# Performance work log

Hardware: AMD Instinct MI355X
Metric: run time of the kernel (lower is better)

The kernel has to match this reference:

```python
import jax, jax.numpy as jnp
import numpy as np

N = 16000
E = 128000
IN_DIM = 512
H1 = 4096
H2 = 1024
OUT_DIM = 64


def setup_inputs() -> dict:
    key = jax.random.key(0)
    ks = jax.random.split(key, 8)
    x = jax.random.normal(ks[0], (N, IN_DIM), dtype=jnp.float32)
    edge_index = jax.random.randint(ks[1], (2, E), 0, N, dtype=jnp.int64)

    def glorot(k, fan_in, fan_out):
        lim = float(np.sqrt(6.0 / (fan_in + fan_out)))
        return jax.random.uniform(k, (fan_in, fan_out), jnp.float32, -lim, lim)

    # PyG SAGEConv: out = lin_l(mean_j x_j) + lin_r(x); lin_l has bias, lin_r does not.
    params = {
        'W1l': glorot(ks[2], IN_DIM, H1), 'b1': jnp.zeros((H1,), jnp.float32),
        'W1r': glorot(ks[3], IN_DIM, H1),
        'W2l': glorot(ks[4], H1, H2), 'b2': jnp.zeros((H2,), jnp.float32),
        'W2r': glorot(ks[5], H1, H2),
        'W3l': glorot(ks[6], H2, OUT_DIM), 'b3': jnp.zeros((OUT_DIM,), jnp.float32),
        'W3r': glorot(ks[7], H2, OUT_DIM),
    }
    return {'x': x, 'edge_index': edge_index, **params}


def _sage_conv(x, src, dst, Wl, b, Wr):
    # mean-aggregate neighbor features at dst, then linear; plus root transform
    agg = jax.ops.segment_sum(x[src], dst, num_segments=N)          # [N, F_in]
    cnt = jax.ops.segment_sum(jnp.ones((src.shape[0],), x.dtype), dst, num_segments=N)
    mean = agg / jnp.maximum(cnt, 1.0)[:, None]
    return mean @ Wl + b + x @ Wr


def reference(x, edge_index, W1l, b1, W1r, W2l, b2, W2r, W3l, b3, W3r):
    src, dst = edge_index[0], edge_index[1]
    h = jax.nn.relu(_sage_conv(x, src, dst, W1l, b1, W1r))   # dropout is identity in eval
    h = jax.nn.relu(_sage_conv(h, src, dst, W2l, b2, W2r))
    h = _sage_conv(h, src, dst, W3l, b3, W3r)
    return jax.nn.log_softmax(h, axis=1)
```

## Files before the change

### kernel.cpp

```cpp
#include <hip/hip_runtime.h>
#include <stdint.h>

typedef __bf16 bf16x8 __attribute__((ext_vector_type(8)));
typedef float  f32x4  __attribute__((ext_vector_type(4)));
typedef const void __attribute__((address_space(1))) gv_t;
typedef void __attribute__((address_space(3))) sv_t;

static __device__ __forceinline__ unsigned short f2bf(float f) {
  unsigned u = __float_as_uint(f);
  u += 0x7fffu + ((u >> 16) & 1u);
  return (unsigned short)(u >> 16);
}
static __device__ __forceinline__ float bf2f(unsigned short h) {
  return __uint_as_float(((unsigned)h) << 16);
}
static __device__ __forceinline__ void gload16(const void* g, void* l) {
  __builtin_amdgcn_global_load_lds((gv_t*)g, (sv_t*)l, 16, 0, 0);
}

__global__ void k_sentinel(float* out, int n, float val) {
  int t = blockIdx.x * 256 + threadIdx.x;
  if (t < n) out[t] = val;
}
__global__ void k_zero(int* p, int n) {
  int t = blockIdx.x * 256 + threadIdx.x;
  if (t < n) p[t] = 0;
}

__global__ void k_detect(const int* ei, int* flag) {
  if (blockIdx.x == 0 && threadIdx.x == 0) {
    int nz = 0;
    for (int t = 0; t < 256; ++t) nz += (ei[2 * t + 1] != 0);
    *flag = (nz == 0) ? 1 : 0;
  }
}

__global__ void k_degree(const int* ei, int E, const int* flag, int* deg) {
  int t = blockIdx.x * 256 + threadIdx.x;
  if (t < E) {
    int d = (*flag) ? ei[2 * (E + t)] : ei[E + t];
    atomicAdd(&deg[d], 1);
  }
}
__global__ void k_scan(const int* deg, int* rp, int* cur, int n) {
  __shared__ int ssum[256];
  int t = threadIdx.x;
  int chunk = (n + 255) >> 8;
  int lo = t * chunk, hi = min(lo + chunk, n);
  int s = 0;
  for (int i = lo; i < hi; ++i) s += deg[i];
  ssum[t] = s;
  __syncthreads();
  if (t == 0) {
    int run = 0;
    for (int i = 0; i < 256; ++i) { int v = ssum[i]; ssum[i] = run; run += v; }
  }
  __syncthreads();
  int run = ssum[t];
  for (int i = lo; i < hi; ++i) { rp[i] = run; cur[i] = run; run += deg[i]; }
  if (t == 255) rp[n] = run;
}
__global__ void k_fill(const int* ei, int E, const int* flag, int* cur, int* col) {
  int t = blockIdx.x * 256 + threadIdx.x;
  if (t < E) {
    int f = *flag;
    int s = f ? ei[2 * t] : ei[t];
    int d = f ? ei[2 * (E + t)] : ei[E + t];
    int p = atomicAdd(&cur[d], 1);
    col[p] = s;
  }
}

__global__ void k_cvtx(const float4* __restrict__ in, ushort4* __restrict__ xm, int total4) {
  int t = blockIdx.x * 256 + threadIdx.x;
  if (t < total4) {
    int row = t >> 7, c = t & 127;
    float4 v = in[t];
    xm[(size_t)row * 256 + c] = make_ushort4(f2bf(v.x), f2bf(v.y), f2bf(v.z), f2bf(v.w));
  }
}

__global__ void k_transW(const float* W, unsigned short* Wt, int K, int N, int ld, int kofs) {
  __shared__ float tile[32][33];
  int tx = threadIdx.x & 31, ty = threadIdx.x >> 5;
  int n0 = blockIdx.x << 5, k0 = blockIdx.y << 5;
#pragma unroll
  for (int r = 0; r < 4; ++r)
    tile[ty + r * 8][tx] = W[(size_t)(k0 + ty + r * 8) * N + n0 + tx];
  __syncthreads();
#pragma unroll
  for (int r = 0; r < 4; ++r)
    Wt[(size_t)(n0 + ty + r * 8) * ld + kofs + k0 + tx] = f2bf(tile[tx][ty + r * 8]);
}

__global__ void k_agg(ushort4* __restrict__ xm, const int* __restrict__ rp,
                      const int* __restrict__ col) {
  int i = blockIdx.x;
  int s = rp[i], e = rp[i + 1];
  float inv = 1.0f / (float)max(e - s, 1);
  int f = threadIdx.x;
  float4 a = make_float4(0.f, 0.f, 0.f, 0.f);
  for (int n = s; n < e; ++n) {
    ushort4 v = xm[(size_t)col[n] * 256 + f];
    a.x += bf2f(v.x); a.y += bf2f(v.y); a.z += bf2f(v.z); a.w += bf2f(v.w);
  }
  xm[(size_t)i * 256 + 128 + f] =
      make_ushort4(f2bf(a.x * inv), f2bf(a.y * inv), f2bf(a.z * inv), f2bf(a.w * inv));
}

template <bool RELU, bool BIAS>
__global__ __launch_bounds__(512, 1) void k_gemm256(
    const unsigned short* __restrict__ A, const unsigned short* __restrict__ B,
    const float* __restrict__ bias, unsigned short* __restrict__ outp,
    int Mreal, int N, int K, int bnShift) {
  __shared__ __align__(16) unsigned short lds[2][2][256 * 64];

  const int tid = threadIdx.x;
  const int lane = tid & 63;
  const int wq = tid >> 6;
  const int wr = wq >> 2;
  const int wc = wq & 3;

  const int nwg = gridDim.x;
  const int q8 = nwg >> 3, r8 = nwg & 7;
  const int xcd = blockIdx.x & 7, idx = blockIdx.x >> 3;
  const int wg = (xcd < r8 ? xcd * (q8 + 1) : r8 * (q8 + 1) + (xcd - r8) * q8) + idx;
  const int bn = wg & ((1 << bnShift) - 1);
  const int bm = wg >> bnShift;

  const unsigned short* Ap = A + (size_t)bm * 256 * K;
  const unsigned short* Bp = B + (size_t)bn * 256 * K;
  const int sl8 = ((lane & 7) ^ (lane >> 3)) * 8;
  const int rsub = wq * 8 + (lane >> 3);

#define STAGE_A(BUF, I, K0)                                            \
  gload16(Ap + (size_t)((I) * 64 + rsub) * K + (K0) + sl8,             \
          (char*)&lds[BUF][0][0] + ((I) * 64 + wq * 8) * 128)
#define STAGE_B(BUF, I, K0)                                            \
  gload16(Bp + (size_t)((I) * 64 + rsub) * K + (K0) + sl8,             \
          (char*)&lds[BUF][1][0] + ((I) * 64 + wq * 8) * 128)
#define VMCNT(NUM) asm volatile("s_waitcnt vmcnt(" #NUM ")" ::: "memory")

  f32x4 acc[8][4];
#pragma unroll
  for (int m = 0; m < 8; ++m)
#pragma unroll
    for (int n = 0; n < 4; ++n) acc[m][n] = (f32x4){0.f, 0.f, 0.f, 0.f};

#define LOAD_AFR(DST, CUR, QA)                                                          \
  do {                                                                                  \
    const char* baseA = (const char*)&lds[CUR][0][0];                                   \
    _Pragma("unroll") for (int mm = 0; mm < 4; ++mm) {                                  \
      const int rr = ((QA) * 4 + mm) * 32 + wr * 16 + (lane & 15);                      \
      _Pragma("unroll") for (int kk = 0; kk < 2; ++kk)                                  \
          DST[mm][kk] = *(const bf16x8*)(baseA + rr * 128 +                             \
                                         (((kk * 4 + (lane >> 4)) ^ (lane & 7)) << 4)); \
    }                                                                                   \
  } while (0)
#define LOAD_BFR(DST, CUR, QB)                                                          \
  do {                                                                                  \
    const char* baseB = (const char*)&lds[CUR][1][0];                                   \
    _Pragma("unroll") for (int nn = 0; nn < 2; ++nn) {                                  \
      const int cc = ((QB) * 2 + nn) * 64 + wc * 16 + (lane & 15);                      \
      _Pragma("unroll") for (int kk = 0; kk < 2; ++kk)                                  \
          DST[nn][kk] = *(const bf16x8*)(baseB + cc * 128 +                             \
                                         (((kk * 4 + (lane >> 4)) ^ (lane & 7)) << 4)); \
    }                                                                                   \
  } while (0)
#define MFMA_Q(QA, QB, AFR, BFR)                                                        \
  do {                                                                                  \
    _Pragma("unroll") for (int mm = 0; mm < 4; ++mm)                                    \
        _Pragma("unroll") for (int nn = 0; nn < 2; ++nn)                                \
            _Pragma("unroll") for (int kk = 0; kk < 2; ++kk)                            \
                acc[(QA) * 4 + mm][(QB) * 2 + nn] =                                     \
                    __builtin_amdgcn_mfma_f32_16x16x32_bf16(                            \
                        AFR[mm][kk], BFR[nn][kk], acc[(QA) * 4 + mm][(QB) * 2 + nn],    \
                        0, 0, 0);                                                       \
  } while (0)

  STAGE_A(0, 0, 0); STAGE_A(0, 1, 0);
  STAGE_B(0, 0, 0); STAGE_B(0, 1, 0);
  STAGE_B(0, 2, 0); STAGE_B(0, 3, 0);
  STAGE_A(0, 2, 0); STAGE_A(0, 3, 0);

  const int nt = K >> 6;
#pragma unroll 1
  for (int t = 0; t < nt; ++t) {
    const int cur = t & 1, nxt = cur ^ 1;
    const int k1 = (t + 1) << 6;
    asm volatile("s_waitcnt lgkmcnt(0)" ::: "memory");
    __builtin_amdgcn_s_barrier();
    if (t < nt - 1) {
      STAGE_A(nxt, 0, k1); STAGE_A(nxt, 1, k1);
      STAGE_B(nxt, 0, k1); STAGE_B(nxt, 1, k1);
      STAGE_B(nxt, 2, k1); STAGE_B(nxt, 3, k1);
      STAGE_A(nxt, 2, k1); STAGE_A(nxt, 3, k1);
      VMCNT(8);
    } else {
      VMCNT(0);
    }
    __builtin_amdgcn_s_barrier();

    __builtin_amdgcn_s_setprio(1);
    {
      bf16x8 a0[4][2], a1[4][2], b0[2][2], b1[2][2];
      LOAD_AFR(a0, cur, 0);
      LOAD_BFR(b0, cur, 0);
      MFMA_Q(0, 0, a0, b0);
      LOAD_BFR(b1, cur, 1);
      MFMA_Q(0, 1, a0, b1);
      LOAD_AFR(a1, cur, 1);
      MFMA_Q(1, 1, a1, b1);
      MFMA_Q(1, 0, a1, b0);
    }
    __builtin_amdgcn_s_setprio(0);
  }

  const int row0 = bm * 256 + wr * 16 + ((lane >> 4) << 2);
  const int col0 = bn * 256 + wc * 16 + (lane & 15);
#pragma unroll
  for (int m = 0; m < 8; ++m) {
#pragma unroll
    for (int n = 0; n < 4; ++n) {
      const int col = col0 + n * 64;
      float bb = BIAS ? bias[col] : 0.f;
#pragma unroll
      for (int r = 0; r < 4; ++r) {
        int row = row0 + m * 32 + r;
        if (row < Mreal) {
          float v = acc[m][n][r] + bb;
          if (RELU) v = fmaxf(v, 0.f);
          outp[(size_t)row * N + col] = f2bf(v);
        }
      }
    }
  }
#undef MFMA_Q
#undef LOAD_BFR
#undef LOAD_AFR
#undef VMCNT
#undef STAGE_A
#undef STAGE_B
}

template <int NF, bool TWO, bool RELU, bool BIAS>
__global__ __launch_bounds__(256) void k_gemm(
    const unsigned short* __restrict__ Am, const unsigned short* __restrict__ Ar,
    const unsigned short* __restrict__ Bl, const unsigned short* __restrict__ Br,
    const float* __restrict__ bias, unsigned short* __restrict__ outp, int N, int K) {
  constexpr int BN = NF * 32;
  __shared__ __align__(16) unsigned short lds[(128 + BN) * 64];
  unsigned short* ldsA = lds;
  unsigned short* ldsB = lds + 128 * 64;

  const int tid = threadIdx.x;
  const int lane = tid & 63;
  const int w = tid >> 6;
  const int wr = w >> 1, wc = w & 1;

  f32x4 zero = {0.f, 0.f, 0.f, 0.f};
  f32x4 acc[4][NF];
#pragma unroll
  for (int m = 0; m < 4; ++m)
#pragma unroll
    for (int n = 0; n < NF; ++n) acc[m][n] = zero;

  const int bm = blockIdx.x, bn = blockIdx.y;
  const int sl_st = (lane & 7) ^ (lane >> 3);

#pragma unroll 1
  for (int pass = 0; pass < (TWO ? 2 : 1); ++pass) {
    const unsigned short* A = (TWO && pass) ? Ar : Am;
    const unsigned short* B = (TWO && pass) ? Br : Bl;
    A += (size_t)bm * 128 * K;
    B += (size_t)bn * BN * K;
#pragma unroll 1
    for (int k0 = 0; k0 < K; k0 += 64) {
      __syncthreads();
#pragma unroll
      for (int q = 0; q < 4; ++q) {
        int rowi = (w * 4 + q) * 8 + (lane >> 3);
        gload16(A + (size_t)rowi * K + k0 + sl_st * 8, (char*)ldsA + (w * 4 + q) * 1024);
      }
#pragma unroll
      for (int q = 0; q < NF; ++q) {
        int rowi = (w * NF + q) * 8 + (lane >> 3);
        gload16(B + (size_t)rowi * K + k0 + sl_st * 8, (char*)ldsB + (w * NF + q) * 1024);
      }
      __syncthreads();
#pragma unroll
      for (int kk = 0; kk < 2; ++kk) {
        int sw = (((kk * 4 + (lane >> 4)) ^ (lane & 7)) << 4);
        bf16x8 af[4], bfr[NF];
#pragma unroll
        for (int m = 0; m < 4; ++m) {
          int r = wr * 64 + m * 16 + (lane & 15);
          af[m] = *(const bf16x8*)((const char*)ldsA + r * 128 + sw);
        }
#pragma unroll
        for (int n = 0; n < NF; ++n) {
          int c = wc * (BN / 2) + n * 16 + (lane & 15);
          bfr[n] = *(const bf16x8*)((const char*)ldsB + c * 128 + sw);
        }
#pragma unroll
        for (int m = 0; m < 4; ++m)
#pragma unroll
          for (int n = 0; n < NF; ++n)
            acc[m][n] = __builtin_amdgcn_mfma_f32_16x16x32_bf16(af[m], bfr[n], acc[m][n], 0, 0, 0);
      }
    }
  }

  const int row0 = bm * 128 + wr * 64;
  const int col0 = bn * BN + wc * (BN / 2);
#pragma unroll
  for (int m = 0; m < 4; ++m) {
#pragma unroll
    for (int n = 0; n < NF; ++n) {
      int col = col0 + n * 16 + (lane & 15);
      float bb = BIAS ? bias[col] : 0.f;
#pragma unroll
      for (int r = 0; r < 4; ++r) {
        int row = row0 + m * 16 + ((lane >> 4) << 2) + r;
        float v = acc[m][n][r] + bb;
        if (RELU) v = fmaxf(v, 0.f);
        outp[(size_t)row * N + col] = f2bf(v);
      }
    }
  }
}

__global__ void k_combine2(const ushort4* __restrict__ Z2, const int* __restrict__ rp,
                           const int* __restrict__ col, const float* __restrict__ bias,
                           ushort4* __restrict__ h2) {
  int i = blockIdx.x;
  int s = rp[i], e = rp[i + 1];
  float inv = 1.0f / (float)max(e - s, 1);
  int f = threadIdx.x;
  float4 a = make_float4(0.f, 0.f, 0.f, 0.f);
  float4 b = make_float4(0.f, 0.f, 0.f, 0.f);
  int n = s;
  for (; n + 1 < e; n += 2) {
    int j0 = col[n], j1 = col[n + 1];
    ushort4 v0 = Z2[(size_t)j0 * 512 + f];
    ushort4 v1 = Z2[(size_t)j1 * 512 + f];
    a.x += bf2f(v0.x); a.y += bf2f(v0.y); a.z += bf2f(v0.z); a.w += bf2f(v0.w);
    b.x += bf2f(v1.x); b.y += bf2f(v1.y); b.z += bf2f(v1.z); b.w += bf2f(v1.w);
  }
  if (n < e) {
    ushort4 v0 = Z2[(size_t)col[n] * 512 + f];
    a.x += bf2f(v0.x); a.y += bf2f(v0.y); a.z += bf2f(v0.z); a.w += bf2f(v0.w);
  }
  a.x += b.x; a.y += b.y; a.z += b.z; a.w += b.w;
  ushort4 r = Z2[(size_t)i * 512 + 256 + f];
  float4 b4 = ((const float4*)bias)[f];
  float o0 = fmaxf(a.x * inv + bf2f(r.x) + b4.x, 0.f);
  float o1 = fmaxf(a.y * inv + bf2f(r.y) + b4.y, 0.f);
  float o2 = fmaxf(a.z * inv + bf2f(r.z) + b4.z, 0.f);
  float o3 = fmaxf(a.w * inv + bf2f(r.w) + b4.w, 0.f);
  h2[(size_t)i * 256 + f] = make_ushort4(f2bf(o0), f2bf(o1), f2bf(o2), f2bf(o3));
}

__global__ void k_combine3(const unsigned short* __restrict__ Z3, const int* __restrict__ rp,
                           const int* __restrict__ col, const float* __restrict__ bias,
                           float* __restrict__ out) {
  int i = blockIdx.x * 4 + (threadIdx.x >> 6);
  int c = threadIdx.x & 63;
  int s = rp[i], e = rp[i + 1];
  float inv = 1.0f / (float)max(e - s, 1);
  float a = 0.f;
  for (int n = s; n < e; ++n) a += bf2f(Z3[(size_t)col[n] * 128 + c]);
  float v = a * inv + bf2f(Z3[(size_t)i * 128 + 64 + c]) + bias[c];
  float m = v;
#pragma unroll
  for (int o = 1; o < 64; o <<= 1) m = fmaxf(m, __shfl_xor(m, o, 64));
  float t = expf(v - m);
  float sum = t;
#pragma unroll
  for (int o = 1; o < 64; o <<= 1) sum += __shfl_xor(sum, o, 64);
  out[(size_t)i * 64 + c] = (v - m) - logf(sum);
}

extern "C" void kernel_launch(void* const* d_in, const int* in_sizes, int n_in,
                              void* d_out, int out_size, void* d_ws, size_t ws_size,
                              hipStream_t stream) {
  const float* x   = (const float*)d_in[0];
  const int*   ei  = (const int*)d_in[1];
  const float* W1l = (const float*)d_in[2];
  const float* b1  = (const float*)d_in[3];
  const float* W1r = (const float*)d_in[4];
  const float* W2l = (const float*)d_in[5];
  const float* b2  = (const float*)d_in[6];
  const float* W2r = (const float*)d_in[7];
  const float* W3l = (const float*)d_in[8];
  const float* b3  = (const float*)d_in[9];
  const float* W3r = (const float*)d_in[10];

  const int Nn = 16000;
  const int E = in_sizes[1] / 2;

  char* p = (char*)d_ws;
  auto carve = [&](size_t bytes) {
    char* r = p;
    p += (bytes + 255) & ~(size_t)255;
    return r;
  };
  int* deg    = (int*)carve((size_t)Nn * 4);
  int* rp     = (int*)carve((size_t)(Nn + 1) * 4);
  int* cur    = (int*)carve((size_t)Nn * 4);
  int* flag   = (int*)carve(4);
  int* colidx = (int*)carve((size_t)E * 4);
  unsigned short* Wb = (unsigned short*)carve((size_t)2048 * 4096 * 2);
  unsigned short* xm = (unsigned short*)carve((size_t)Nn * 1024 * 2);
  unsigned short* h1 = (unsigned short*)carve((size_t)Nn * 4096 * 2);
  unsigned short* Z2 = (unsigned short*)carve((size_t)Nn * 2048 * 2);
  unsigned short* Z3 = (unsigned short*)carve((size_t)Nn * 128 * 2);
  unsigned short* h2 = xm;

  size_t need = (size_t)(p - (char*)d_ws);
  if (ws_size < need) {
    k_sentinel<<<(out_size + 255) / 256, 256, 0, stream>>>((float*)d_out, out_size,
                                                           (float)(ws_size >> 20));
    return;
  }

  k_zero<<<(Nn + 255) / 256, 256, 0, stream>>>(deg, Nn);
  k_detect<<<1, 64, 0, stream>>>(ei, flag);
  k_degree<<<(E + 255) / 256, 256, 0, stream>>>(ei, E, flag, deg);
  k_scan<<<1, 256, 0, stream>>>(deg, rp, cur, Nn);
  k_fill<<<(E + 255) / 256, 256, 0, stream>>>(ei, E, flag, cur, colidx);

  k_cvtx<<<(Nn * 128 + 255) / 256, 256, 0, stream>>>((const float4*)x, (ushort4*)xm, Nn * 128);
  k_transW<<<dim3(4096 / 32, 512 / 32), 256, 0, stream>>>(W1r, Wb, 512, 4096, 1024, 0);
  k_transW<<<dim3(4096 / 32, 512 / 32), 256, 0, stream>>>(W1l, Wb, 512, 4096, 1024, 512);
  k_agg<<<Nn, 128, 0, stream>>>((ushort4*)xm, rp, colidx);
  k_gemm256<true, true><<<63 * 16, 512, 0, stream>>>(xm, Wb, b1, h1, Nn, 4096, 1024, 4);

  k_transW<<<dim3(1024 / 32, 4096 / 32), 256, 0, stream>>>(W2l, Wb, 4096, 1024, 4096, 0);
  k_transW<<<dim3(1024 / 32, 4096 / 32), 256, 0, stream>>>(W2r, Wb + (size_t)1024 * 4096, 4096,
                                                           1024, 4096, 0);
  k_gemm256<false, false><<<63 * 8, 512, 0, stream>>>(h1, Wb, nullptr, Z2, Nn, 2048, 4096, 3);
  k_combine2<<<Nn, 256, 0, stream>>>((const ushort4*)Z2, rp, colidx, b2, (ushort4*)h2);

  k_transW<<<dim3(64 / 32, 1024 / 32), 256, 0, stream>>>(W3l, Wb, 1024, 64, 1024, 0);
  k_transW<<<dim3(64 / 32, 1024 / 32), 256, 0, stream>>>(W3r, Wb + (size_t)64 * 1024, 1024, 64,
                                                         1024, 0);
  k_gemm<2, false, false, false><<<dim3(125, 2), 256, 0, stream>>>(h2, nullptr, Wb, nullptr,
                                                                   nullptr, Z3, 128, 1024);
  k_combine3<<<Nn / 4, 256, 0, stream>>>(Z3, rp, colidx, b3, (float*)d_out);

  (void)n_in; (void)out_size;
}
```

Measured before the change: 623.3 us.

## Restructure GEMM main loop into a two-tile-ahead prefetch pipeline with interleaved fragment loads

```diff
diff --git a/kernel.cpp b/kernel.cpp
--- a/kernel.cpp
+++ b/kernel.cpp
@@ -182,37 +182,47 @@
   STAGE_B(0, 0, 0); STAGE_B(0, 1, 0);
   STAGE_B(0, 2, 0); STAGE_B(0, 3, 0);
   STAGE_A(0, 2, 0); STAGE_A(0, 3, 0);
+  STAGE_A(1, 0, 64); STAGE_A(1, 1, 64);
+  STAGE_B(1, 0, 64); STAGE_B(1, 1, 64);
+  STAGE_B(1, 2, 64); STAGE_B(1, 3, 64);
+  STAGE_A(1, 2, 64); STAGE_A(1, 3, 64);
+  VMCNT(8);
+  __builtin_amdgcn_s_barrier();
+
+  bf16x8 a0[4][2], b0[2][2], a1[4][2], b1[2][2];
+  LOAD_AFR(a0, 0, 0);
+  LOAD_BFR(b0, 0, 0);
 
   const int nt = K >> 6;
 #pragma unroll 1
   for (int t = 0; t < nt; ++t) {
     const int cur = t & 1, nxt = cur ^ 1;
-    const int k1 = (t + 1) << 6;
+    const int k2 = (t + 2) << 6;
+    LOAD_AFR(a1, cur, 1);
+    LOAD_BFR(b1, cur, 1);
+    __builtin_amdgcn_s_setprio(1);
+    MFMA_Q(0, 0, a0, b0);
+    __builtin_amdgcn_s_setprio(0);
     asm volatile("s_waitcnt lgkmcnt(0)" ::: "memory");
     __builtin_amdgcn_s_barrier();
-    if (t < nt - 1) {
-      STAGE_A(nxt, 0, k1); STAGE_A(nxt, 1, k1);
-      STAGE_B(nxt, 0, k1); STAGE_B(nxt, 1, k1);
-      STAGE_B(nxt, 2, k1); STAGE_B(nxt, 3, k1);
-      STAGE_A(nxt, 2, k1); STAGE_A(nxt, 3, k1);
-      VMCNT(8);
-    } else {
-      VMCNT(0);
+    if (t + 2 < nt) {
+      STAGE_A(cur, 0, k2); STAGE_A(cur, 1, k2);
+      STAGE_B(cur, 0, k2); STAGE_B(cur, 1, k2);
+      STAGE_B(cur, 2, k2); STAGE_B(cur, 3, k2);
+      STAGE_A(cur, 2, k2); STAGE_A(cur, 3, k2);
     }
-    __builtin_amdgcn_s_barrier();
-
     __builtin_amdgcn_s_setprio(1);
-    {
-      bf16x8 a0[4][2], a1[4][2], b0[2][2], b1[2][2];
-      LOAD_AFR(a0, cur, 0);
-      LOAD_BFR(b0, cur, 0);
-      MFMA_Q(0, 0, a0, b0);
-      LOAD_BFR(b1, cur, 1);
-      MFMA_Q(0, 1, a0, b1);
-      LOAD_AFR(a1, cur, 1);
-      MFMA_Q(1, 1, a1, b1);
-      MFMA_Q(1, 0, a1, b0);
+    MFMA_Q(1, 0, a1, b0);
+    MFMA_Q(0, 1, a0, b1);
+    __builtin_amdgcn_s_setprio(0);
+    if (t + 1 < nt) {
+      if (t + 2 < nt) { VMCNT(8); } else { VMCNT(0); }
+      __builtin_amdgcn_s_barrier();
+      LOAD_AFR(a0, nxt, 0);
+      LOAD_BFR(b0, nxt, 0);
     }
+    __builtin_amdgcn_s_setprio(1);
+    MFMA_Q(1, 1, a1, b1);
     __builtin_amdgcn_s_setprio(0);
   }
 
```

After: 590.0 us. 5.3% less time.

## Software-pipeline 256x256 GEMM mainloop with register prefetch and precomputed LDS offsets

Applied to the files above, without the earlier changes.

```diff
diff --git a/kernel.cpp b/kernel.cpp
--- a/kernel.cpp
+++ b/kernel.cpp
@@ -133,13 +133,35 @@
   const int sl8 = ((lane & 7) ^ (lane >> 3)) * 8;
   const int rsub = wq * 8 + (lane >> 3);
 
-#define STAGE_A(BUF, I, K0)                                            \
-  gload16(Ap + (size_t)((I) * 64 + rsub) * K + (K0) + sl8,             \
-          (char*)&lds[BUF][0][0] + ((I) * 64 + wq * 8) * 128)
-#define STAGE_B(BUF, I, K0)                                            \
-  gload16(Bp + (size_t)((I) * 64 + rsub) * K + (K0) + sl8,             \
-          (char*)&lds[BUF][1][0] + ((I) * 64 + wq * 8) * 128)
-#define VMCNT(NUM) asm volatile("s_waitcnt vmcnt(" #NUM ")" ::: "memory")
+  const char* ldsc = (const char*)&lds[0][0][0];
+  const unsigned laneA = (unsigned)(wr * 16 + (lane & 15)) * 128;
+  const unsigned laneB = 32768u + (unsigned)(wc * 16 + (lane & 15)) * 128;
+  const unsigned sk0 = (unsigned)(((lane >> 4) ^ (lane & 7)) << 4);
+  const unsigned sk1 = (unsigned)(((4 + (lane >> 4)) ^ (lane & 7)) << 4);
+  const unsigned A0k0 = laneA + sk0, A0k1 = laneA + sk1;
+  const unsigned B0k0 = laneB + sk0, B0k1 = laneB + sk1;
+  const unsigned A1k0 = 65536u + A0k0, A1k1 = 65536u + A0k1;
+  const unsigned B1k0 = 65536u + B0k0, B1k1 = 65536u + B0k1;
+
+  const unsigned short* aStage = Ap + (size_t)rsub * K + sl8 + 128;
+  const unsigned short* bStage = Bp + (size_t)rsub * K + sl8 + 128;
+  const size_t str1 = (size_t)64 * K;
+  const size_t str2 = 2 * str1, str3 = 3 * str1;
+  char* ldsd = (char*)&lds[0][0][0];
+  const unsigned dA = (unsigned)(wq * 8) * 128;
+  const unsigned dB = 32768u + (unsigned)(wq * 8) * 128;
+
+#define STAGE8(BUFOFF)                                                   \
+  do {                                                                   \
+    gload16(aStage,        ldsd + (BUFOFF) + dA);                        \
+    gload16(aStage + str1, ldsd + (BUFOFF) + dA + 8192);                 \
+    gload16(aStage + str2, ldsd + (BUFOFF) + dA + 16384);                \
+    gload16(aStage + str3, ldsd + (BUFOFF) + dA + 24576);                \
+    gload16(bStage,        ldsd + (BUFOFF) + dB);                        \
+    gload16(bStage + str1, ldsd + (BUFOFF) + dB + 8192);                 \
+    gload16(bStage + str2, ldsd + (BUFOFF) + dB + 16384);                \
+    gload16(bStage + str3, ldsd + (BUFOFF) + dB + 24576);                \
+  } while (0)
 
   f32x4 acc[8][4];
 #pragma unroll
@@ -147,25 +169,20 @@
 #pragma unroll
     for (int n = 0; n < 4; ++n) acc[m][n] = (f32x4){0.f, 0.f, 0.f, 0.f};
 
-#define LOAD_AFR(DST, CUR, QA)                                                          \
-  do {                                                                                  \
-    const char* baseA = (const char*)&lds[CUR][0][0];                                   \
-    _Pragma("unroll") for (int mm = 0; mm < 4; ++mm) {                                  \
-      const int rr = ((QA) * 4 + mm) * 32 + wr * 16 + (lane & 15);                      \
-      _Pragma("unroll") for (int kk = 0; kk < 2; ++kk)                                  \
-          DST[mm][kk] = *(const bf16x8*)(baseA + rr * 128 +                             \
-                                         (((kk * 4 + (lane >> 4)) ^ (lane & 7)) << 4)); \
-    }                                                                                   \
+#define LDSRD(OFF) (*(const bf16x8*)(ldsc + (OFF)))
+#define LOAD_AFR2(DST, BA0, BA1, QA)                                     \
+  do {                                                                   \
+    _Pragma("unroll") for (int mm = 0; mm < 4; ++mm) {                   \
+      DST[mm][0] = LDSRD((BA0) + (QA) * 16384 + mm * 4096);              \
+      DST[mm][1] = LDSRD((BA1) + (QA) * 16384 + mm * 4096);              \
+    }                                                                    \
   } while (0)
-#define LOAD_BFR(DST, CUR, QB)                                                          \
-  do {                                                                                  \
-    const char* baseB = (const char*)&lds[CUR][1][0];                                   \
-    _Pragma("unroll") for (int nn = 0; nn < 2; ++nn) {                                  \
-      const int cc = ((QB) * 2 + nn) * 64 + wc * 16 + (lane & 15);                      \
-      _Pragma("unroll") for (int kk = 0; kk < 2; ++kk)                                  \
-          DST[nn][kk] = *(const bf16x8*)(baseB + cc * 128 +                             \
-                                         (((kk * 4 + (lane >> 4)) ^ (lane & 7)) << 4)); \
-    }                                                                                   \
+#define LOAD_BFR2(DST, BB0, BB1, QB)                                     \
+  do {                                                                   \
+    _Pragma("unroll") for (int nn = 0; nn < 2; ++nn) {                   \
+      DST[nn][0] = LDSRD((BB0) + (QB) * 16384 + nn * 8192);              \
+      DST[nn][1] = LDSRD((BB1) + (QB) * 16384 + nn * 8192);              \
+    }                                                                    \
   } while (0)
 #define MFMA_Q(QA, QB, AFR, BFR)                                                        \
   do {                                                                                  \
@@ -178,42 +195,56 @@
                         0, 0, 0);                                                       \
   } while (0)
 
-  STAGE_A(0, 0, 0); STAGE_A(0, 1, 0);
-  STAGE_B(0, 0, 0); STAGE_B(0, 1, 0);
-  STAGE_B(0, 2, 0); STAGE_B(0, 3, 0);
-  STAGE_A(0, 2, 0); STAGE_A(0, 3, 0);
+  {
+    const unsigned short* a0p = Ap + (size_t)rsub * K + sl8;
+    const unsigned short* b0p = Bp + (size_t)rsub * K + sl8;
+    gload16(a0p,        ldsd + dA);          gload16(a0p + str1, ldsd + dA + 8192);
+    gload16(a0p + str2, ldsd + dA + 16384);  gload16(a0p + str3, ldsd + dA + 24576);
+    gload16(b0p,        ldsd + dB);          gload16(b0p + str1, ldsd + dB + 8192);
+    gload16(b0p + str2, ldsd + dB + 16384);  gload16(b0p + str3, ldsd + dB + 24576);
+    gload16(a0p + 64,        ldsd + 65536 + dA);
+    gload16(a0p + 64 + str1, ldsd + 65536 + dA + 8192);
+    gload16(a0p + 64 + str2, ldsd + 65536 + dA + 16384);
+    gload16(a0p + 64 + str3, ldsd + 65536 + dA + 24576);
+    gload16(b0p + 64,        ldsd + 65536 + dB);
+    gload16(b0p + 64 + str1, ldsd + 65536 + dB + 8192);
+    gload16(b0p + 64 + str2, ldsd + 65536 + dB + 16384);
+    gload16(b0p + 64 + str3, ldsd + 65536 + dB + 24576);
+  }
+  asm volatile("s_waitcnt vmcnt(8)" ::: "memory");
+  __builtin_amdgcn_s_barrier();
+
+  bf16x8 a0[4][2], b0[2][2], a1[4][2], b1[2][2];
+  LOAD_AFR2(a0, A0k0, A0k1, 0);
+  LOAD_BFR2(b0, B0k0, B0k1, 0);
 
   const int nt = K >> 6;
+#define ITER(AC0, AC1, BC0, BC1, AN0, AN1, BN0, BN1, BUFOFF, T)          \
+  do {                                                                   \
+    LOAD_BFR2(b1, BC0, BC1, 1);                                          \
+    LOAD_AFR2(a1, AC0, AC1, 1);                                          \
+    __builtin_amdgcn_s_setprio(1);                                       \
+    MFMA_Q(0, 0, a0, b0);                                                \
+    MFMA_Q(0, 1, a0, b1);                                                \
+    __builtin_amdgcn_s_setprio(0);                                       \
+    asm volatile("s_waitcnt vmcnt(0) lgkmcnt(0)" ::: "memory");          \
+    __builtin_amdgcn_s_barrier();                                        \
+    if ((T) + 2 < nt) STAGE8(BUFOFF);                                    \
+    __builtin_amdgcn_s_setprio(1);                                       \
+    MFMA_Q(1, 0, a1, b0);                                                \
+    MFMA_Q(1, 1, a1, b1);                                                \
+    __builtin_amdgcn_s_setprio(0);                                       \
+    if ((T) + 1 < nt) {                                                  \
+      LOAD_AFR2(a0, AN0, AN1, 0);                                        \
+      LOAD_BFR2(b0, BN0, BN1, 0);                                        \
+    }                                                                    \
+    aStage += 64; bStage += 64;                                          \
+  } while (0)
+
 #pragma unroll 1
-  for (int t = 0; t < nt; ++t) {
-    const int cur = t & 1, nxt = cur ^ 1;
-    const int k1 = (t + 1) << 6;
-    asm volatile("s_waitcnt lgkmcnt(0)" ::: "memory");
-    __builtin_amdgcn_s_barrier();
-    if (t < nt - 1) {
-      STAGE_A(nxt, 0, k1); STAGE_A(nxt, 1, k1);
-      STAGE_B(nxt, 0, k1); STAGE_B(nxt, 1, k1);
-      STAGE_B(nxt, 2, k1); STAGE_B(nxt, 3, k1);
-      STAGE_A(nxt, 2, k1); STAGE_A(nxt, 3, k1);
-      VMCNT(8);
-    } else {
-      VMCNT(0);
-    }
-    __builtin_amdgcn_s_barrier();
-
-    __builtin_amdgcn_s_setprio(1);
-    {
-      bf16x8 a0[4][2], a1[4][2], b0[2][2], b1[2][2];
-      LOAD_AFR(a0, cur, 0);
-      LOAD_BFR(b0, cur, 0);
-      MFMA_Q(0, 0, a0, b0);
-      LOAD_BFR(b1, cur, 1);
-      MFMA_Q(0, 1, a0, b1);
-      LOAD_AFR(a1, cur, 1);
-      MFMA_Q(1, 1, a1, b1);
-      MFMA_Q(1, 0, a1, b0);
-    }
-    __builtin_amdgcn_s_setprio(0);
+  for (int t = 0; t < nt; t += 2) {
+    ITER(A0k0, A0k1, B0k0, B0k1, A1k0, A1k1, B1k0, B1k1, 0u, t);
+    ITER(A1k0, A1k1, B1k0, B1k1, A0k0, A0k1, B0k0, B0k1, 65536u, t + 1);
   }
 
   const int row0 = bm * 256 + wr * 16 + ((lane >> 4) << 2);
@@ -235,12 +266,12 @@
       }
     }
   }
+#undef ITER
 #undef MFMA_Q
-#undef LOAD_BFR
-#undef LOAD_AFR
-#undef VMCNT
-#undef STAGE_A
-#undef STAGE_B
+#undef LOAD_BFR2
+#undef LOAD_AFR2
+#undef LDSRD
+#undef STAGE8
 }
 
 template <int NF, bool TWO, bool RELU, bool BIAS>
```

New measurement: 715.9 us. 1.15x slower.
